# Performance work log

Measured on AMD Instinct MI355X. Metric: run time of the kernel, lower is better.

The kernel has to match this reference:

```python
import jax, jax.numpy as jnp
import numpy as np

B, H, S, D = 2, 16, 2048, 64

def setup_inputs() -> dict:
    key = jax.random.key(0)
    kq, kk, kv = jax.random.split(key, 3)
    query = jax.random.normal(kq, (B, H, S, D), dtype=jnp.float32)
    k_ = jax.random.normal(kk, (B, H, S, D), dtype=jnp.float32)
    value = jax.random.normal(kv, (B, H, S, D), dtype=jnp.float32)
    # causal 0/1 mask, broadcasts over batch/head dims
    mask = jnp.tril(jnp.ones((S, S), dtype=jnp.float32))
    return {"query": query, "key": k_, "value": value, "mask": mask}

def reference(query, key, value, mask):
    scale = 1.0 / jnp.sqrt(jnp.asarray(query.shape[-1], query.dtype))
    # [B,H,Sq,Sk] score matrix (naive, fully materialized like the original)
    scores = jnp.einsum('bhqd,bhkd->bhqk', query, key) * scale
    scores = jnp.where(mask == 0, -jnp.inf, scores)
    attn = jax.nn.softmax(scores, axis=-1)
    return jnp.einsum('bhqk,bhkd->bhqd', attn, value)
```

## Files before the change

### kernel.cpp

```cpp
#include <hip/hip_runtime.h>
#include <hip/hip_bf16.h>
#include <math.h>

typedef __attribute__((ext_vector_type(4)))  float f32x4;
typedef __attribute__((ext_vector_type(16))) float f32x16;
typedef __attribute__((ext_vector_type(8)))  short bf16x8;
typedef __attribute__((ext_vector_type(4)))  short bf16x4;

#define S_SZ 2048
#define D_SZ 64

constexpr int KVBLK = 64;
constexpr int KP  = 72;
constexpr int NQT = 16;
constexpr float SCL2 = 0.18033688011112042f;
constexpr float DEFER_THR = 44.0f;

struct Smem {
    short Kt[2][KVBLK][KP];
    short Vt[2][4096];
};
union SmemU {
    Smem s;
    struct {
        float Om[128][66];
        float Mm[2][128];
        float Lm[2][128];
    } e;
};

__device__ __forceinline__ short f2bf(float f) {
    union { __hip_bfloat16 h; short s; } u;
    u.h = __float2bfloat16(f);
    return u.s;
}
__device__ __forceinline__ unsigned cvt_pk_bf16(float lo, float hi) {
    unsigned r;
    asm("v_cvt_pk_bf16_f32 %0, %1, %2" : "=v"(r) : "v"(lo), "v"(hi));
    return r;
}
#define PSWAP(a, b) asm("v_permlane32_swap_b32 %0, %1" : "+v"(a), "+v"(b))
#define TRREAD(dst, addr, off) \
    asm volatile("ds_read_b64_tr_b16 %0, %1 offset:" #off : "=v"(dst) : "v"(addr))

__device__ __forceinline__ bf16x8 cat(bf16x4 a, bf16x4 b) {
    return __builtin_shufflevector(a, b, 0, 1, 2, 3, 4, 5, 6, 7);
}

__global__ __launch_bounds__(512, 2)
void attn_fwd(const float* __restrict__ Q, const float* __restrict__ K,
              const float* __restrict__ V, float* __restrict__ O)
{
    __shared__ __align__(16) SmemU u;
    Smem* sm = &u.s;

    const int tid  = threadIdx.x;
    const int wid  = tid >> 6;
    const int lane = tid & 63;
    const int lq   = lane & 31;
    const int h    = lane >> 5;
    const int grp  = wid >> 2;
    const int wq   = wid & 3;

    const int b    = blockIdx.x;
    const int pass = b >> 8;
    const int c    = b & 255;
    const int xcd  = c & 7;
    const int i2   = c >> 3;
    const int j    = i2 & 7;
    const int head = xcd + 8 * (i2 >> 3);
    const int qt   = pass ? j : (NQT - 1 - j);

    const int qbase = qt * 128 + wq * 32;
    const int qglob = qbase + lq;
    const int nT    = 2 * qt + 2;

    const size_t hoff = (size_t)head * S_SZ * D_SZ;
    const float* Qh = Q + hoff;
    const float* Kh = K + hoff;
    const float* Vh = V + hoff;
    float*       Oh = O + hoff;

    const int kr  = tid >> 3;
    const int kc0 = (tid & 7) * 8;
    const int vt_off = (((tid & 7) >> 1) * 16 + (kr >> 2)) * 64
                     + (kr & 3) * 16 + (tid & 1) * 8;

    const int cg = (lane >> 4) & 1;
    const unsigned vtbase = (unsigned)(uintptr_t)&sm->Vt[0][0]
                          + (unsigned)cg * 2048u + (unsigned)grp * 1024u
                          + (unsigned)h * 256u + (unsigned)(lane & 15) * 8u;

    bf16x8 qfrag[4];
    {
        const float* qrow = Qh + (size_t)qglob * D_SZ;
        #pragma unroll
        for (int dc = 0; dc < 4; ++dc) {
            const float* ptr = qrow + dc * 16 + h * 8;
            f32x4 a0 = *(const f32x4*)ptr;
            f32x4 a1 = *(const f32x4*)(ptr + 4);
            bf16x8 q;
            q[0]=f2bf(a0[0]); q[1]=f2bf(a0[1]); q[2]=f2bf(a0[2]); q[3]=f2bf(a0[3]);
            q[4]=f2bf(a1[0]); q[5]=f2bf(a1[1]); q[6]=f2bf(a1[2]); q[7]=f2bf(a1[3]);
            qfrag[dc] = q;
        }
    }

    f32x16 oa0, oa1;
    #pragma unroll
    for (int r = 0; r < 16; ++r) { oa0[r] = 0.f; oa1[r] = 0.f; }
    float m_run = -INFINITY, l_run = 0.f;

    f32x4 kreg[2], vreg[2];

    {
        const float* ksrc = Kh + (size_t)kr * D_SZ + kc0;
        const float* vsrc = Vh + (size_t)kr * D_SZ + kc0;
        kreg[0] = ((const f32x4*)ksrc)[0]; kreg[1] = ((const f32x4*)ksrc)[1];
        vreg[0] = ((const f32x4*)vsrc)[0]; vreg[1] = ((const f32x4*)vsrc)[1];
    }
    {
        bf16x8 p0;
        p0[0]=f2bf(kreg[0][0]); p0[1]=f2bf(kreg[0][1]); p0[2]=f2bf(kreg[0][2]); p0[3]=f2bf(kreg[0][3]);
        p0[4]=f2bf(kreg[1][0]); p0[5]=f2bf(kreg[1][1]); p0[6]=f2bf(kreg[1][2]); p0[7]=f2bf(kreg[1][3]);
        *(bf16x8*)&sm->Kt[0][kr][kc0] = p0;
        bf16x8 v0;
        v0[0]=f2bf(vreg[0][0]); v0[1]=f2bf(vreg[0][1]); v0[2]=f2bf(vreg[0][2]); v0[3]=f2bf(vreg[0][3]);
        v0[4]=f2bf(vreg[1][0]); v0[5]=f2bf(vreg[1][1]); v0[6]=f2bf(vreg[1][2]); v0[7]=f2bf(vreg[1][3]);
        *(bf16x8*)&sm->Vt[0][vt_off] = v0;
    }
    __syncthreads();

    for (int t = 0; t < nT; ++t) {
        const int buf = t & 1;
        const int kmin = 64 * t + grp * 32;
        const bool active = kmin <= qbase + 31;

        if (t + 1 < nT) {
            const float* ksrc = Kh + (size_t)((t + 1) * KVBLK + kr) * D_SZ + kc0;
            const float* vsrc = Vh + (size_t)((t + 1) * KVBLK + kr) * D_SZ + kc0;
            kreg[0] = ((const f32x4*)ksrc)[0]; kreg[1] = ((const f32x4*)ksrc)[1];
            vreg[0] = ((const f32x4*)vsrc)[0]; vreg[1] = ((const f32x4*)vsrc)[1];
        }

        if (active) {
            f32x16 st0;
            #pragma unroll
            for (int r = 0; r < 16; ++r) st0[r] = 0.f;
            __builtin_amdgcn_s_setprio(1);
            #pragma unroll
            for (int dc = 0; dc < 4; ++dc) {
                bf16x8 kf0 = *(const bf16x8*)&sm->Kt[buf][grp * 32 + lq][dc * 16 + h * 8];
                st0 = __builtin_amdgcn_mfma_f32_32x32x16_bf16(kf0, qfrag[dc], st0, 0, 0, 0);
            }
            __builtin_amdgcn_s_setprio(0);

            const unsigned va = vtbase + (buf ? 8192u : 0u);
            bf16x4 t00, t01, t10, t11;
            bf16x4 u00, u01, u10, u11;
            TRREAD(t00, va, 0);    TRREAD(t01, va, 128);
            TRREAD(t10, va, 512);  TRREAD(t11, va, 640);
            TRREAD(u00, va, 4096); TRREAD(u01, va, 4224);
            TRREAD(u10, va, 4608); TRREAD(u11, va, 4736);

            if (kmin + 31 > qbase) {
                #pragma unroll
                for (int r = 0; r < 16; ++r) {
                    const int k0 = kmin + (r & 3) + 8 * (r >> 2) + 4 * h;
                    if (k0 > qglob) st0[r] = -INFINITY;
                }
            }

            float px0 = -INFINITY, px1 = -INFINITY, px2 = -INFINITY, px3 = -INFINITY;
            #pragma unroll
            for (int r = 0; r < 4; ++r) {
                px0 = fmaxf(px0, st0[4*r]);
                px1 = fmaxf(px1, st0[4*r+1]);
                px2 = fmaxf(px2, st0[4*r+2]);
                px3 = fmaxf(px3, st0[4*r+3]);
            }
            float pmax = fmaxf(fmaxf(px0, px1), fmaxf(px2, px3));
            pmax = fmaxf(pmax, __shfl_xor(pmax, 32));

            if (!__all(pmax - m_run <= DEFER_THR)) {
                const float mnew  = fmaxf(m_run, pmax);
                const float alpha = __builtin_amdgcn_exp2f((m_run - mnew) * SCL2);
                m_run = mnew;
                l_run *= alpha;
                #pragma unroll
                for (int r = 0; r < 16; ++r) { oa0[r] *= alpha; oa1[r] *= alpha; }
            }
            const float mb = m_run * SCL2;

            float ps0 = 0.f, ps1 = 0.f, ps2 = 0.f, ps3 = 0.f;
            #pragma unroll
            for (int r = 0; r < 4; ++r) {
                st0[4*r]   = __builtin_amdgcn_exp2f(fmaf(st0[4*r],   SCL2, -mb));
                st0[4*r+1] = __builtin_amdgcn_exp2f(fmaf(st0[4*r+1], SCL2, -mb));
                st0[4*r+2] = __builtin_amdgcn_exp2f(fmaf(st0[4*r+2], SCL2, -mb));
                st0[4*r+3] = __builtin_amdgcn_exp2f(fmaf(st0[4*r+3], SCL2, -mb));
                ps0 += st0[4*r];
                ps1 += st0[4*r+1];
                ps2 += st0[4*r+2];
                ps3 += st0[4*r+3];
            }
            float psum = (ps0 + ps1) + (ps2 + ps3);
            psum += __shfl_xor(psum, 32);
            l_run += psum;

            bf16x8 pfrag[2];
            {
                unsigned w0, w1, w2, w3;
                w0 = cvt_pk_bf16(st0[0], st0[1]);   w1 = cvt_pk_bf16(st0[2], st0[3]);
                w2 = cvt_pk_bf16(st0[4], st0[5]);   w3 = cvt_pk_bf16(st0[6], st0[7]);
                PSWAP(w0, w2); PSWAP(w1, w3);
                { union { unsigned uu[4]; bf16x8 v; } ww = {{w0, w1, w2, w3}}; pfrag[0] = ww.v; }
                w0 = cvt_pk_bf16(st0[8], st0[9]);   w1 = cvt_pk_bf16(st0[10], st0[11]);
                w2 = cvt_pk_bf16(st0[12], st0[13]); w3 = cvt_pk_bf16(st0[14], st0[15]);
                PSWAP(w0, w2); PSWAP(w1, w3);
                { union { unsigned uu[4]; bf16x8 v; } ww = {{w0, w1, w2, w3}}; pfrag[1] = ww.v; }
            }

            asm volatile("s_waitcnt lgkmcnt(0)" ::: "memory");
            __builtin_amdgcn_sched_barrier(0);

            __builtin_amdgcn_s_setprio(1);
            oa0 = __builtin_amdgcn_mfma_f32_32x32x16_bf16(cat(t00, t01), pfrag[0], oa0, 0, 0, 0);
            oa0 = __builtin_amdgcn_mfma_f32_32x32x16_bf16(cat(t10, t11), pfrag[1], oa0, 0, 0, 0);
            oa1 = __builtin_amdgcn_mfma_f32_32x32x16_bf16(cat(u00, u01), pfrag[0], oa1, 0, 0, 0);
            oa1 = __builtin_amdgcn_mfma_f32_32x32x16_bf16(cat(u10, u11), pfrag[1], oa1, 0, 0, 0);
            __builtin_amdgcn_s_setprio(0);
        }

        if (t + 1 < nT) {
            const int nb = buf ^ 1;
            bf16x8 p0;
            p0[0]=f2bf(kreg[0][0]); p0[1]=f2bf(kreg[0][1]); p0[2]=f2bf(kreg[0][2]); p0[3]=f2bf(kreg[0][3]);
            p0[4]=f2bf(kreg[1][0]); p0[5]=f2bf(kreg[1][1]); p0[6]=f2bf(kreg[1][2]); p0[7]=f2bf(kreg[1][3]);
            *(bf16x8*)&sm->Kt[nb][kr][kc0] = p0;
            bf16x8 v0;
            v0[0]=f2bf(vreg[0][0]); v0[1]=f2bf(vreg[0][1]); v0[2]=f2bf(vreg[0][2]); v0[3]=f2bf(vreg[0][3]);
            v0[4]=f2bf(vreg[1][0]); v0[5]=f2bf(vreg[1][1]); v0[6]=f2bf(vreg[1][2]); v0[7]=f2bf(vreg[1][3]);
            *(bf16x8*)&sm->Vt[nb][vt_off] = v0;
        }
        __syncthreads();
    }

    const int qv = wq * 32 + lq;
    if (h == 0) { u.e.Mm[grp][qv] = m_run; u.e.Lm[grp][qv] = l_run; }
    __syncthreads();
    {
        const float mA = u.e.Mm[0][qv], mB = u.e.Mm[1][qv];
        const float lA = u.e.Lm[0][qv], lB = u.e.Lm[1][qv];
        const float mX = fmaxf(mA, mB);
        const float aA = __builtin_amdgcn_exp2f((mA - mX) * SCL2);
        const float aB = __builtin_amdgcn_exp2f((mB - mX) * SCL2);
        const float linv = 1.f / (lA * aA + lB * aB);
        const float scl = (grp ? aB : aA) * linv;

        if (grp == 0) {
            #pragma unroll
            for (int s = 0; s < 4; ++s) {
                f32x4 w0, w1;
                #pragma unroll
                for (int j2 = 0; j2 < 4; ++j2) { w0[j2] = oa0[4*s+j2] * scl; w1[j2] = oa1[4*s+j2] * scl; }
                *(f32x4*)&u.e.Om[qv][     s * 8 + 4 * h] = w0;
                *(f32x4*)&u.e.Om[qv][32 + s * 8 + 4 * h] = w1;
            }
        }
        __syncthreads();
        if (grp == 1) {
            #pragma unroll
            for (int s = 0; s < 4; ++s) {
                f32x4 w0 = *(const f32x4*)&u.e.Om[qv][     s * 8 + 4 * h];
                f32x4 w1 = *(const f32x4*)&u.e.Om[qv][32 + s * 8 + 4 * h];
                #pragma unroll
                for (int j2 = 0; j2 < 4; ++j2) { w0[j2] += oa0[4*s+j2] * scl; w1[j2] += oa1[4*s+j2] * scl; }
                *(f32x4*)&u.e.Om[qv][     s * 8 + 4 * h] = w0;
                *(f32x4*)&u.e.Om[qv][32 + s * 8 + 4 * h] = w1;
            }
        }
        __syncthreads();
    }

    {
        const int row = tid >> 2;
        const int c0  = (tid & 3) * 16;
        float* dst = Oh + (size_t)(qt * 128 + row) * D_SZ + c0;
        const float* src = &u.e.Om[row][c0];
        #pragma unroll
        for (int j2 = 0; j2 < 4; ++j2)
            ((f32x4*)dst)[j2] = ((const f32x4*)src)[j2];
    }
}

extern "C" void kernel_launch(void* const* d_in, const int* in_sizes, int n_in,
                              void* d_out, int out_size, void* d_ws, size_t ws_size,
                              hipStream_t stream) {
    const float* Q = (const float*)d_in[0];
    const float* K = (const float*)d_in[1];
    const float* V = (const float*)d_in[2];
    float* Ou = (float*)d_out;
    attn_fwd<<<dim3(512), 512, 0, stream>>>(Q, K, V, Ou);
}
```

Baseline: 47.28 us.

## Widen blocks to four KV groups and pair causal q-tiles per block

```diff
diff --git a/kernel.cpp b/kernel.cpp
--- a/kernel.cpp
+++ b/kernel.cpp
@@ -10,7 +10,7 @@
 #define S_SZ 2048
 #define D_SZ 64
 
-constexpr int KVBLK = 64;
+constexpr int KVBLK = 128;
 constexpr int KP  = 72;
 constexpr int NQT = 16;
 constexpr float SCL2 = 0.18033688011112042f;
@@ -18,14 +18,15 @@
 
 struct Smem {
     short Kt[2][KVBLK][KP];
-    short Vt[2][4096];
+    short Vt[2][8192];
 };
 union SmemU {
     Smem s;
     struct {
-        float Om[128][66];
-        float Mm[2][128];
-        float Lm[2][128];
+        float Om1[128][68];
+        float Om2[128][68];
+        float Mm[4][128];
+        float Lm[4][128];
     } e;
 };
 
@@ -47,49 +48,20 @@
     return __builtin_shufflevector(a, b, 0, 1, 2, 3, 4, 5, 6, 7);
 }
 
-__global__ __launch_bounds__(512, 2)
-void attn_fwd(const float* __restrict__ Q, const float* __restrict__ K,
-              const float* __restrict__ V, float* __restrict__ O)
+__device__ __forceinline__ void process_qtile(
+    int qt, const float* __restrict__ Qh, const float* __restrict__ Kh,
+    const float* __restrict__ Vh, float* __restrict__ Oh, SmemU& u,
+    int tid, int lq, int h, int grp, int wq, unsigned vtbase)
 {
-    __shared__ __align__(16) SmemU u;
     Smem* sm = &u.s;
-
-    const int tid  = threadIdx.x;
-    const int wid  = tid >> 6;
-    const int lane = tid & 63;
-    const int lq   = lane & 31;
-    const int h    = lane >> 5;
-    const int grp  = wid >> 2;
-    const int wq   = wid & 3;
-
-    const int b    = blockIdx.x;
-    const int pass = b >> 8;
-    const int c    = b & 255;
-    const int xcd  = c & 7;
-    const int i2   = c >> 3;
-    const int j    = i2 & 7;
-    const int head = xcd + 8 * (i2 >> 3);
-    const int qt   = pass ? j : (NQT - 1 - j);
-
     const int qbase = qt * 128 + wq * 32;
     const int qglob = qbase + lq;
-    const int nT    = 2 * qt + 2;
-
-    const size_t hoff = (size_t)head * S_SZ * D_SZ;
-    const float* Qh = Q + hoff;
-    const float* Kh = K + hoff;
-    const float* Vh = V + hoff;
-    float*       Oh = O + hoff;
+    const int nT    = qt + 1;
 
     const int kr  = tid >> 3;
     const int kc0 = (tid & 7) * 8;
-    const int vt_off = (((tid & 7) >> 1) * 16 + (kr >> 2)) * 64
+    const int vt_off = (((tid & 7) >> 1) * 32 + (kr >> 2)) * 64
                      + (kr & 3) * 16 + (tid & 1) * 8;
-
-    const int cg = (lane >> 4) & 1;
-    const unsigned vtbase = (unsigned)(uintptr_t)&sm->Vt[0][0]
-                          + (unsigned)cg * 2048u + (unsigned)grp * 1024u
-                          + (unsigned)h * 256u + (unsigned)(lane & 15) * 8u;
 
     bf16x8 qfrag[4];
     {
@@ -119,6 +91,7 @@
         kreg[0] = ((const f32x4*)ksrc)[0]; kreg[1] = ((const f32x4*)ksrc)[1];
         vreg[0] = ((const f32x4*)vsrc)[0]; vreg[1] = ((const f32x4*)vsrc)[1];
     }
+    __syncthreads();
     {
         bf16x8 p0;
         p0[0]=f2bf(kreg[0][0]); p0[1]=f2bf(kreg[0][1]); p0[2]=f2bf(kreg[0][2]); p0[3]=f2bf(kreg[0][3]);
@@ -133,7 +106,7 @@
 
     for (int t = 0; t < nT; ++t) {
         const int buf = t & 1;
-        const int kmin = 64 * t + grp * 32;
+        const int kmin = 128 * t + 32 * grp;
         const bool active = kmin <= qbase + 31;
 
         if (t + 1 < nT) {
@@ -155,13 +128,13 @@
             }
             __builtin_amdgcn_s_setprio(0);
 
-            const unsigned va = vtbase + (buf ? 8192u : 0u);
+            const unsigned va = vtbase + (buf ? 16384u : 0u);
             bf16x4 t00, t01, t10, t11;
             bf16x4 u00, u01, u10, u11;
             TRREAD(t00, va, 0);    TRREAD(t01, va, 128);
             TRREAD(t10, va, 512);  TRREAD(t11, va, 640);
-            TRREAD(u00, va, 4096); TRREAD(u01, va, 4224);
-            TRREAD(u10, va, 4608); TRREAD(u11, va, 4736);
+            TRREAD(u00, va, 8192); TRREAD(u01, va, 8320);
+            TRREAD(u10, va, 8704); TRREAD(u11, va, 8832);
 
             if (kmin + 31 > qbase) {
                 #pragma unroll
@@ -251,47 +224,88 @@
     __syncthreads();
     {
         const float mA = u.e.Mm[0][qv], mB = u.e.Mm[1][qv];
+        const float mC = u.e.Mm[2][qv], mD = u.e.Mm[3][qv];
         const float lA = u.e.Lm[0][qv], lB = u.e.Lm[1][qv];
-        const float mX = fmaxf(mA, mB);
+        const float lC = u.e.Lm[2][qv], lD = u.e.Lm[3][qv];
+        const float mX = fmaxf(fmaxf(mA, mB), fmaxf(mC, mD));
         const float aA = __builtin_amdgcn_exp2f((mA - mX) * SCL2);
         const float aB = __builtin_amdgcn_exp2f((mB - mX) * SCL2);
-        const float linv = 1.f / (lA * aA + lB * aB);
-        const float scl = (grp ? aB : aA) * linv;
-
-        if (grp == 0) {
+        const float aC = __builtin_amdgcn_exp2f((mC - mX) * SCL2);
+        const float aD = __builtin_amdgcn_exp2f((mD - mX) * SCL2);
+        const float linv = 1.f / (lA * aA + lB * aB + lC * aC + lD * aD);
+        const float ag = (grp == 0) ? aA : (grp == 1) ? aB : (grp == 2) ? aC : aD;
+        const float scl = ag * linv;
+        float (*Om)[68] = (grp < 2) ? u.e.Om1 : u.e.Om2;
+
+        if ((grp & 1) == 0) {
             #pragma unroll
             for (int s = 0; s < 4; ++s) {
                 f32x4 w0, w1;
                 #pragma unroll
                 for (int j2 = 0; j2 < 4; ++j2) { w0[j2] = oa0[4*s+j2] * scl; w1[j2] = oa1[4*s+j2] * scl; }
-                *(f32x4*)&u.e.Om[qv][     s * 8 + 4 * h] = w0;
-                *(f32x4*)&u.e.Om[qv][32 + s * 8 + 4 * h] = w1;
+                *(f32x4*)&Om[qv][     s * 8 + 4 * h] = w0;
+                *(f32x4*)&Om[qv][32 + s * 8 + 4 * h] = w1;
             }
         }
         __syncthreads();
-        if (grp == 1) {
+        if ((grp & 1) == 1) {
             #pragma unroll
             for (int s = 0; s < 4; ++s) {
-                f32x4 w0 = *(const f32x4*)&u.e.Om[qv][     s * 8 + 4 * h];
-                f32x4 w1 = *(const f32x4*)&u.e.Om[qv][32 + s * 8 + 4 * h];
+                f32x4 w0 = *(const f32x4*)&Om[qv][     s * 8 + 4 * h];
+                f32x4 w1 = *(const f32x4*)&Om[qv][32 + s * 8 + 4 * h];
                 #pragma unroll
                 for (int j2 = 0; j2 < 4; ++j2) { w0[j2] += oa0[4*s+j2] * scl; w1[j2] += oa1[4*s+j2] * scl; }
-                *(f32x4*)&u.e.Om[qv][     s * 8 + 4 * h] = w0;
-                *(f32x4*)&u.e.Om[qv][32 + s * 8 + 4 * h] = w1;
+                *(f32x4*)&Om[qv][     s * 8 + 4 * h] = w0;
+                *(f32x4*)&Om[qv][32 + s * 8 + 4 * h] = w1;
             }
         }
         __syncthreads();
     }
 
     {
-        const int row = tid >> 2;
-        const int c0  = (tid & 3) * 16;
+        const int row = tid >> 3;
+        const int c0  = (tid & 7) * 8;
         float* dst = Oh + (size_t)(qt * 128 + row) * D_SZ + c0;
-        const float* src = &u.e.Om[row][c0];
-        #pragma unroll
-        for (int j2 = 0; j2 < 4; ++j2)
-            ((f32x4*)dst)[j2] = ((const f32x4*)src)[j2];
-    }
+        f32x4 r0 = *(const f32x4*)&u.e.Om1[row][c0]     + *(const f32x4*)&u.e.Om2[row][c0];
+        f32x4 r1 = *(const f32x4*)&u.e.Om1[row][c0 + 4] + *(const f32x4*)&u.e.Om2[row][c0 + 4];
+        ((f32x4*)dst)[0] = r0;
+        ((f32x4*)dst)[1] = r1;
+    }
+}
+
+__global__ __launch_bounds__(1024, 4)
+void attn_fwd(const float* __restrict__ Q, const float* __restrict__ K,
+              const float* __restrict__ V, float* __restrict__ O)
+{
+    __shared__ __align__(16) SmemU u;
+
+    const int tid  = threadIdx.x;
+    const int wid  = tid >> 6;
+    const int lane = tid & 63;
+    const int lq   = lane & 31;
+    const int h    = lane >> 5;
+    const int grp  = wid >> 2;
+    const int wq   = wid & 3;
+
+    const int b    = blockIdx.x;
+    const int xcd  = b & 7;
+    const int i2   = b >> 3;
+    const int p    = i2 & 7;
+    const int head = xcd + 8 * (i2 >> 3);
+
+    const size_t hoff = (size_t)head * S_SZ * D_SZ;
+    const float* Qh = Q + hoff;
+    const float* Kh = K + hoff;
+    const float* Vh = V + hoff;
+    float*       Oh = O + hoff;
+
+    const int cg = (lane >> 4) & 1;
+    const unsigned vtbase = (unsigned)(uintptr_t)&u.s.Vt[0][0]
+                          + (unsigned)cg * 4096u + (unsigned)grp * 1024u
+                          + (unsigned)h * 256u + (unsigned)(lane & 15) * 8u;
+
+    process_qtile(p,           Qh, Kh, Vh, Oh, u, tid, lq, h, grp, wq, vtbase);
+    process_qtile(NQT - 1 - p, Qh, Kh, Vh, Oh, u, tid, lq, h, grp, wq, vtbase);
 }
 
 extern "C" void kernel_launch(void* const* d_in, const int* in_sizes, int n_in,
@@ -301,5 +315,5 @@
     const float* K = (const float*)d_in[1];
     const float* V = (const float*)d_in[2];
     float* Ou = (float*)d_out;
-    attn_fwd<<<dim3(512), 512, 0, stream>>>(Q, K, V, Ou);
-}
+    attn_fwd<<<dim3(256), 1024, 0, stream>>>(Q, K, V, Ou);
+}
```

Measured after the change: 53.00 us. 1.12x slower.
